# Kernel tuning notes

Measured on AMD Instinct MI355X. Metric: run time of the kernel, lower is better.

## Reference

```python
import jax, jax.numpy as jnp
import numpy as np

B, CM, CT, CA, H, W = 4, 256, 64, 128, 80, 80


def setup_inputs() -> dict:
    key = jax.random.key(0)
    ks = jax.random.split(key, 10)
    s = lambda fan_in: 1.0 / np.sqrt(fan_in)
    return {
        "met_features": jax.random.normal(ks[0], (B, CM, H, W), jnp.float32),
        "terrain_features": jax.random.normal(ks[1], (B, CT, H, W), jnp.float32),
        "wq": jax.random.normal(ks[2], (CA, CM), jnp.float32) * s(CM),
        "bq": jax.random.normal(ks[3], (CA,), jnp.float32) * s(CM),
        "wk": jax.random.normal(ks[4], (CA, CT), jnp.float32) * s(CT),
        "bk": jax.random.normal(ks[5], (CA,), jnp.float32) * s(CT),
        "wv": jax.random.normal(ks[6], (CA, CT), jnp.float32) * s(CT),
        "bv": jax.random.normal(ks[7], (CA,), jnp.float32) * s(CT),
        "wo": jax.random.normal(ks[8], (CM, CA), jnp.float32) * s(CA),
        "bo": jax.random.normal(ks[9], (CM,), jnp.float32) * s(CA),
    }


def reference(met_features, terrain_features, wq, bq, wk, bk, wv, bv, wo, bo):
    b, c, h, w = met_features.shape
    n = h * w  # tokens
    scale = CA ** (-0.5)
    # 1x1 convs == per-pixel linear: [B,Cin,N] -> [B,Cattn,N]
    met = met_features.reshape(b, c, n)
    ter = terrain_features.reshape(b, terrain_features.shape[1], n)
    q = jnp.einsum('oc,bcn->bon', wq, met) + bq[None, :, None]
    k = jnp.einsum('oc,bcn->bon', wk, ter) + bk[None, :, None]
    v = jnp.einsum('oc,bcn->bon', wv, ter) + bv[None, :, None]
    # attn[b, i, j] = sum_c q[b,c,i] * k[b,c,j]
    attn = jax.nn.softmax(jnp.einsum('bci,bcj->bij', q, k) * scale, axis=-1)
    # out[b, c, i] = sum_j v[b,c,j] * attn[b,i,j]
    out = jnp.einsum('bcj,bij->bci', v, attn)
    out = jnp.einsum('oc,bcn->bon', wo, out) + bo[None, :, None]
    return met_features + out.reshape(b, c, h, w)
```

## Files before the change

kernel.cpp:

```cpp
#include <hip/hip_runtime.h>
#include <hip/hip_bf16.h>

#define BB 4
#define CMv 256
#define CTv 64
#define CAv 128
#define NTOK 6400
#define KVSPLIT 5
#define KVRANGE 1280
#define NTILES 20
#define QSCL 0.12753102198064644f

typedef unsigned short u16;
typedef __attribute__((ext_vector_type(8))) short sh8;
typedef __attribute__((ext_vector_type(4))) float f32x4;
typedef __attribute__((ext_vector_type(16))) float f32x16;
typedef __attribute__((ext_vector_type(4))) unsigned uint4v;
typedef __attribute__((ext_vector_type(2))) unsigned uint2v;

__device__ __forceinline__ u16 f2bf(float f) {
  return __builtin_bit_cast(u16, __float2bfloat16(f));
}
__device__ __forceinline__ float bf2f(u16 x) {
  unsigned u = ((unsigned)x) << 16;
  return __builtin_bit_cast(float, u);
}
__device__ __forceinline__ unsigned pk2(float a, float b) {
  return ((unsigned)f2bf(b) << 16) | (unsigned)f2bf(a);
}
__device__ __forceinline__ f32x16 zero16() {
  f32x16 z;
#pragma unroll
  for (int i = 0; i < 16; i++) z[i] = 0.f;
  return z;
}
typedef const __attribute__((address_space(1))) unsigned int* gas_p;
typedef __attribute__((address_space(3))) unsigned int* las_p;
__device__ __forceinline__ void gl_lds16(const u16* g, u16* l) {
  __builtin_amdgcn_global_load_lds((gas_p)g, (las_p)l, 16, 0, 0);
}

__global__ __launch_bounds__(256) void prep(const float* __restrict__ wq,
                                            const float* __restrict__ bq,
                                            const float* __restrict__ wk,
                                            const float* __restrict__ wv,
                                            const float* __restrict__ wo,
                                            u16* __restrict__ wqB,
                                            float* __restrict__ bqs,
                                            u16* __restrict__ wkB,
                                            u16* __restrict__ wvB,
                                            u16* __restrict__ woB) {
  const int i0 = blockIdx.x * 256 + threadIdx.x;
  const int stride = gridDim.x * 256;
  for (int i = i0; i < 128 * 256; i += stride) wqB[i] = f2bf(wq[i] * QSCL);
  for (int i = i0; i < 128 * 64; i += stride) { wkB[i] = f2bf(wk[i]); wvB[i] = f2bf(wv[i]); }
  for (int i = i0; i < 256 * 128; i += stride) woB[i] = f2bf(wo[i]);
  for (int i = i0; i < 128; i += stride) bqs[i] = bq[i] * QSCL;
}

__global__ __launch_bounds__(512, 2) void qkvproj(const float* __restrict__ met,
                                                  const float* __restrict__ ter,
                                                  const u16* __restrict__ wqB,
                                                  const float* __restrict__ bqs,
                                                  const u16* __restrict__ wkB,
                                                  const float* __restrict__ bk,
                                                  const u16* __restrict__ wvB,
                                                  const float* __restrict__ bv,
                                                  u16* __restrict__ Qtm,
                                                  u16* __restrict__ Ktm,
                                                  u16* __restrict__ Vcm) {
  const int tid = threadIdx.x;
  const int w = tid >> 6;
  const int lane = tid & 63;
  const int l31 = lane & 31;
  const int h = lane >> 5;

  if (blockIdx.x < 200) {
    const int b = blockIdx.x / 50;
    const int tokb = (blockIdx.x % 50) * 128;
    const int chg = (w & 3) * 32;
    const int half = w >> 2;
    const u16* wb = wqB + (size_t)(chg + l31) * 256 + h * 8;
    sh8 af[16];
#pragma unroll
    for (int kk = 0; kk < 16; kk++) af[kk] = *(const sh8*)(wb + kk * 16);
    float bias[16];
#pragma unroll
    for (int r = 0; r < 16; r++) bias[r] = bqs[chg + (r & 3) + 8 * (r >> 2) + 4 * h];
    const float* mp = met + (size_t)b * CMv * NTOK;
#pragma unroll
    for (int ct = 0; ct < 2; ct++) {
      const int tok = tokb + (half * 2 + ct) * 32 + l31;
      f32x16 acc = zero16();
#pragma unroll
      for (int kk = 0; kk < 16; kk++) {
        const float* cp = mp + (size_t)(kk * 16 + 8 * h) * NTOK + tok;
        float x0 = cp[0], x1 = cp[(size_t)NTOK], x2 = cp[(size_t)2 * NTOK],
              x3 = cp[(size_t)3 * NTOK], x4 = cp[(size_t)4 * NTOK],
              x5 = cp[(size_t)5 * NTOK], x6 = cp[(size_t)6 * NTOK],
              x7 = cp[(size_t)7 * NTOK];
        uint4v u = {pk2(x0, x1), pk2(x2, x3), pk2(x4, x5), pk2(x6, x7)};
        acc = __builtin_amdgcn_mfma_f32_32x32x16_bf16(
            af[kk], __builtin_bit_cast(sh8, u), acc, 0, 0, 0);
      }
      u16* qp = Qtm + ((size_t)b * NTOK + tok) * CAv;
#pragma unroll
      for (int rq = 0; rq < 4; rq++) {
        const int ch0 = chg + 8 * rq + 4 * h;
        uint2v d = {pk2(acc[4 * rq + 0] + bias[4 * rq + 0],
                        acc[4 * rq + 1] + bias[4 * rq + 1]),
                    pk2(acc[4 * rq + 2] + bias[4 * rq + 2],
                        acc[4 * rq + 3] + bias[4 * rq + 3])};
        *(uint2v*)(qp + ch0) = d;
      }
    }
  } else {
    const int bx = blockIdx.x - 200;
    const int b = bx / 50;
    const int tokb = (bx % 50) * 128;
    const bool isV = w >= 4;
    const int chg = (w & 3) * 32;
    const u16* wb = (isV ? wvB : wkB) + (size_t)(chg + l31) * 64 + h * 8;
    sh8 af[4];
#pragma unroll
    for (int kk = 0; kk < 4; kk++) af[kk] = *(const sh8*)(wb + kk * 16);
    const float* barr = isV ? bv : bk;
    float bias[16];
#pragma unroll
    for (int r = 0; r < 16; r++) bias[r] = barr[chg + (r & 3) + 8 * (r >> 2) + 4 * h];
    const float* tp = ter + (size_t)b * CTv * NTOK;
#pragma unroll
    for (int ct = 0; ct < 4; ct++) {
      const int tok = tokb + ct * 32 + l31;
      f32x16 acc = zero16();
#pragma unroll
      for (int kk = 0; kk < 4; kk++) {
        const float* cp = tp + (size_t)(kk * 16 + 8 * h) * NTOK + tok;
        float x0 = cp[0], x1 = cp[(size_t)NTOK], x2 = cp[(size_t)2 * NTOK],
              x3 = cp[(size_t)3 * NTOK], x4 = cp[(size_t)4 * NTOK],
              x5 = cp[(size_t)5 * NTOK], x6 = cp[(size_t)6 * NTOK],
              x7 = cp[(size_t)7 * NTOK];
        uint4v u = {pk2(x0, x1), pk2(x2, x3), pk2(x4, x5), pk2(x6, x7)};
        acc = __builtin_amdgcn_mfma_f32_32x32x16_bf16(
            af[kk], __builtin_bit_cast(sh8, u), acc, 0, 0, 0);
      }
      if (!isV) {
        u16* kp = Ktm + ((size_t)b * NTOK + tok) * CAv;
#pragma unroll
        for (int rq = 0; rq < 4; rq++) {
          const int ch0 = chg + 8 * rq + 4 * h;
          uint2v d = {pk2(acc[4 * rq + 0] + bias[4 * rq + 0],
                          acc[4 * rq + 1] + bias[4 * rq + 1]),
                      pk2(acc[4 * rq + 2] + bias[4 * rq + 2],
                          acc[4 * rq + 3] + bias[4 * rq + 3])};
          *(uint2v*)(kp + ch0) = d;
        }
      } else {
#pragma unroll
        for (int r = 0; r < 16; r++) {
          const int ch = chg + (r & 3) + 8 * (r >> 2) + 4 * h;
          Vcm[((size_t)b * CAv + ch) * NTOK + tok] = f2bf(acc[r] + bias[r]);
        }
      }
    }
  }
}

__global__ __launch_bounds__(512, 2) void attn(const u16* __restrict__ Qtm,
                                               const u16* __restrict__ Ktm,
                                               const u16* __restrict__ Vcm,
                                               u16* __restrict__ Opart,
                                               float* __restrict__ Lpart) {
  __shared__ __align__(16) unsigned char smem[65536];

  const int tid = threadIdx.x;
  const int w = tid >> 6;
  const int lane = tid & 63;
  const int l31 = lane & 31;
  const int h = lane >> 5;

  const int g = blockIdx.x % 20;
  const int qt = blockIdx.x / 20;
  const int b = g / KVSPLIT;
  const int kvq = g % KVSPLIT;
  const int qb0 = qt * 256;
  const int kv00 = kvq * KVRANGE;

  const u16* Qb = Qtm + ((size_t)b * NTOK + qb0 + w * 32 + l31) * CAv;
  const u16* Kb = Ktm + (size_t)b * NTOK * CAv;
  const u16* Vb = Vcm + (size_t)b * CAv * NTOK;

  sh8 qf[8];
#pragma unroll
  for (int kk = 0; kk < 8; kk++) qf[kk] = *(const sh8*)(Qb + kk * 16 + h * 8);

  const int kr0 = w * 8 + (lane >> 4);
  const int kr1 = kr0 + 4;
  const u16* ksrc0 = Kb + ((size_t)kv00 + kr0) * CAv + (((lane & 15) ^ (kr0 & 15)) * 8);
  const u16* ksrc1 = Kb + ((size_t)kv00 + kr1) * CAv + (((lane & 15) ^ (kr1 & 15)) * 8);
  const int vc = w * 16 + (lane >> 3);
  const u16* vsrc = Vb + (size_t)vc * NTOK + kv00 +
                    (((lane & 7) ^ ((lane >> 3) & 7)) * 8);

  int koff[8];
#pragma unroll
  for (int kk = 0; kk < 8; kk++)
    koff[kk] = l31 * 256 + (((2 * kk + h) ^ (l31 & 15)) << 4);
  int voff[4];
#pragma unroll
  for (int b2 = 0; b2 < 4; b2++)
    voff[b2] = l31 * 128 + (((2 * b2 + h) ^ (l31 & 7)) << 4);

#define STAGE(p)                                               \
  do {                                                         \
    u16* kb_ = (u16*)(smem + (p) * 32768) + w * 1024;          \
    gl_lds16(ksrc0, kb_);                                      \
    gl_lds16(ksrc1, kb_ + 512);                                \
    u16* vb_ = (u16*)(smem + (p) * 32768 + 16384) + w * 1024;  \
    gl_lds16(vsrc, vb_);                                       \
    gl_lds16(vsrc + (size_t)8 * NTOK, vb_ + 512);              \
    ksrc0 += 64 * CAv;                                         \
    ksrc1 += 64 * CAv;                                         \
    vsrc += 64;                                                \
  } while (0)

  STAGE(0);
  asm volatile("s_waitcnt vmcnt(0)" ::: "memory");
  __builtin_amdgcn_s_barrier();

  f32x16 o[4];
#pragma unroll
  for (int i = 0; i < 4; i++) o[i] = zero16();
  float lsum = 0.f;

  int buf = 0;
  for (int t = 0; t < NTILES; t++) {
    if (t < NTILES - 1) STAGE(buf ^ 1);
    const unsigned char* kbuf = smem + buf * 32768;
    const unsigned char* vbuf = kbuf + 16384;
    __builtin_amdgcn_s_setprio(1);
    f32x16 s0 = zero16(), s1 = zero16();
#pragma unroll
    for (int kk = 0; kk < 8; kk++) {
      sh8 kfa = *(const sh8*)(kbuf + koff[kk]);
      sh8 kfb = *(const sh8*)(kbuf + 8192 + koff[kk]);
      s0 = __builtin_amdgcn_mfma_f32_32x32x16_bf16(kfa, qf[kk], s0, 0, 0, 0);
      s1 = __builtin_amdgcn_mfma_f32_32x32x16_bf16(kfb, qf[kk], s1, 0, 0, 0);
    }
    __builtin_amdgcn_s_setprio(0);
    f32x16 p0, p1;
#pragma unroll
    for (int r = 0; r < 16; r++) {
      p0[r] = __builtin_exp2f(s0[r]);
      p1[r] = __builtin_exp2f(s1[r]);
    }
#pragma unroll
    for (int r = 0; r < 16; r++) lsum += p0[r] + p1[r];
    unsigned pkm0[4][2], pkm1[4][2];
#pragma unroll
    for (int rq = 0; rq < 4; rq++) {
      pkm0[rq][0] = pk2(p0[4 * rq + 0], p0[4 * rq + 1]);
      pkm0[rq][1] = pk2(p0[4 * rq + 2], p0[4 * rq + 3]);
      pkm1[rq][0] = pk2(p1[4 * rq + 0], p1[4 * rq + 1]);
      pkm1[rq][1] = pk2(p1[4 * rq + 2], p1[4 * rq + 3]);
    }
#pragma unroll
    for (int x = 0; x < 2; x++) {
#pragma unroll
      for (int b2i = 0; b2i < 2; b2i++) {
        unsigned ow0, ow1, sd0, sd1;
        if (x == 0) {
          ow0 = h ? pkm0[2 * b2i + 1][0] : pkm0[2 * b2i][0];
          ow1 = h ? pkm0[2 * b2i + 1][1] : pkm0[2 * b2i][1];
          sd0 = h ? pkm0[2 * b2i][0] : pkm0[2 * b2i + 1][0];
          sd1 = h ? pkm0[2 * b2i][1] : pkm0[2 * b2i + 1][1];
        } else {
          ow0 = h ? pkm1[2 * b2i + 1][0] : pkm1[2 * b2i][0];
          ow1 = h ? pkm1[2 * b2i + 1][1] : pkm1[2 * b2i][1];
          sd0 = h ? pkm1[2 * b2i][0] : pkm1[2 * b2i + 1][0];
          sd1 = h ? pkm1[2 * b2i][1] : pkm1[2 * b2i + 1][1];
        }
        unsigned rv0 = (unsigned)__shfl_xor((int)sd0, 32);
        unsigned rv1 = (unsigned)__shfl_xor((int)sd1, 32);
        uint4v fw = {h ? rv0 : ow0, h ? rv1 : ow1, h ? ow0 : rv0, h ? ow1 : rv1};
        sh8 pf = __builtin_bit_cast(sh8, fw);
        const int b2 = x * 2 + b2i;
        __builtin_amdgcn_s_setprio(1);
#pragma unroll
        for (int ct = 0; ct < 4; ct++) {
          sh8 vf = *(const sh8*)(vbuf + ct * 4096 + voff[b2]);
          o[ct] = __builtin_amdgcn_mfma_f32_32x32x16_bf16(vf, pf, o[ct], 0, 0, 0);
        }
        __builtin_amdgcn_s_setprio(0);
      }
    }
    asm volatile("s_waitcnt vmcnt(0)" ::: "memory");
    __builtin_amdgcn_s_barrier();
    buf ^= 1;
  }
#undef STAGE

  lsum += __shfl_xor(lsum, 32);
  u16* op = Opart + (((size_t)kvq * BB + b) * NTOK + qb0 + w * 32 + l31) * CAv;
#pragma unroll
  for (int ct = 0; ct < 4; ct++)
#pragma unroll
    for (int rq = 0; rq < 4; rq++) {
      uint2v d = {pk2(o[ct][4 * rq + 0], o[ct][4 * rq + 1]),
                  pk2(o[ct][4 * rq + 2], o[ct][4 * rq + 3])};
      *(uint2v*)(op + ct * 32 + rq * 8 + h * 4) = d;
    }
  if (h == 0) {
    size_t mi = ((size_t)kvq * BB + b) * NTOK + qb0 + w * 32 + l31;
    Lpart[mi] = lsum;
  }
}

__global__ __launch_bounds__(512, 2) void outproj(const float* __restrict__ met,
                                                  const u16* __restrict__ woB,
                                                  const float* __restrict__ bo,
                                                  const u16* __restrict__ Opart,
                                                  const float* __restrict__ Lpart,
                                                  float* __restrict__ out) {
  const int tid = threadIdx.x;
  const int w = tid >> 6;
  const int lane = tid & 63;
  const int l31 = lane & 31;
  const int h = lane >> 5;

  const int b = blockIdx.x / 100;
  const int tokb = (blockIdx.x % 100) * 64;
  const int chg = (w & 3) * 64;
  const int ct = w >> 2;
  const int tok = tokb + ct * 32 + l31;
  const size_t n = (size_t)b * NTOK + tok;
  const size_t PSTR = (size_t)BB * NTOK;

  const u16* wb0 = woB + (size_t)(chg + l31) * 128 + h * 8;
  const u16* wb1 = woB + (size_t)(chg + 32 + l31) * 128 + h * 8;
  sh8 a0[8], a1[8];
#pragma unroll
  for (int kk = 0; kk < 8; kk++) {
    a0[kk] = *(const sh8*)(wb0 + kk * 16);
    a1[kk] = *(const sh8*)(wb1 + kk * 16);
  }

  float L = 0.f;
#pragma unroll
  for (int i = 0; i < KVSPLIT; i++) L += Lpart[i * PSTR + n];
  const float rL = 1.f / L;

  f32x16 acc0 = zero16(), acc1 = zero16();
#pragma unroll
  for (int kk = 0; kk < 8; kk++) {
    float s[8];
#pragma unroll
    for (int j = 0; j < 8; j++) s[j] = 0.f;
#pragma unroll
    for (int i = 0; i < KVSPLIT; i++) {
      sh8 v = *(const sh8*)(Opart + (i * PSTR + n) * CAv + kk * 16 + 8 * h);
#pragma unroll
      for (int j = 0; j < 8; j++) s[j] += bf2f((u16)v[j]);
    }
    uint4v u = {pk2(s[0] * rL, s[1] * rL), pk2(s[2] * rL, s[3] * rL),
                pk2(s[4] * rL, s[5] * rL), pk2(s[6] * rL, s[7] * rL)};
    sh8 bf = __builtin_bit_cast(sh8, u);
    acc0 = __builtin_amdgcn_mfma_f32_32x32x16_bf16(a0[kk], bf, acc0, 0, 0, 0);
    acc1 = __builtin_amdgcn_mfma_f32_32x32x16_bf16(a1[kk], bf, acc1, 0, 0, 0);
  }
#pragma unroll
  for (int r = 0; r < 16; r++) {
    const int ro = (r & 3) + 8 * (r >> 2) + 4 * h;
    const int ch0 = chg + ro;
    const int ch1 = chg + 32 + ro;
    size_t i0 = ((size_t)b * CMv + ch0) * NTOK + tok;
    size_t i1 = ((size_t)b * CMv + ch1) * NTOK + tok;
    out[i0] = met[i0] + acc0[r] + bo[ch0];
    out[i1] = met[i1] + acc1[r] + bo[ch1];
  }
}

extern "C" void kernel_launch(void* const* d_in, const int* in_sizes, int n_in,
                              void* d_out, int out_size, void* d_ws, size_t ws_size,
                              hipStream_t stream) {
  const float* met = (const float*)d_in[0];
  const float* ter = (const float*)d_in[1];
  const float* wq = (const float*)d_in[2];
  const float* bq = (const float*)d_in[3];
  const float* wk = (const float*)d_in[4];
  const float* bk = (const float*)d_in[5];
  const float* wv = (const float*)d_in[6];
  const float* bv = (const float*)d_in[7];
  const float* wo = (const float*)d_in[8];
  const float* bo = (const float*)d_in[9];
  float* out = (float*)d_out;

  u16* Qtm = (u16*)d_ws;
  u16* Ktm = Qtm + (size_t)BB * NTOK * CAv;
  u16* Vcm = Ktm + (size_t)BB * NTOK * CAv;
  u16* Opart = Vcm + (size_t)BB * NTOK * CAv;
  float* Lpart = (float*)(Opart + (size_t)KVSPLIT * BB * NTOK * CAv);
  u16* wqB = (u16*)(Lpart + (size_t)KVSPLIT * BB * NTOK);
  u16* wkB = wqB + 128 * 256;
  u16* wvB = wkB + 128 * 64;
  u16* woB = wvB + 128 * 64;
  float* bqs = (float*)(woB + 256 * 128);

  prep<<<dim3(40), dim3(256), 0, stream>>>(wq, bq, wk, wv, wo, wqB, bqs, wkB, wvB, woB);
  qkvproj<<<dim3(400), dim3(512), 0, stream>>>(met, ter, wqB, bqs, wkB, bk,
                                               wvB, bv, Qtm, Ktm, Vcm);
  attn<<<dim3(500), dim3(512), 0, stream>>>(Qtm, Ktm, Vcm, Opart, Lpart);
  outproj<<<dim3(400), dim3(512), 0, stream>>>(met, woB, bo, Opart, Lpart, out);
}
```

Baseline: 182.3 us.

## Software-pipeline QK^T one tile ahead with triple-buffered K in attention

Restructures the attention loop so the QK^T MFMAs for tile t+1 are issued before the exp/pack/PV work of tile t, letting matrix-core work overlap the softmax VALU work. K is triple-buffered and V double-buffered in LDS, which grows shared memory from 64KB to 80KB. With launch_bounds(512,2), the larger LDS footprint may reduce blocks per CU, and holding an extra pair of score accumulators raises register pressure.

```diff
diff --git a/kernel.cpp b/kernel.cpp
--- a/kernel.cpp
+++ b/kernel.cpp
@@ -171,7 +171,7 @@
                                                const u16* __restrict__ Vcm,
                                                u16* __restrict__ Opart,
                                                float* __restrict__ Lpart) {
-  __shared__ __align__(16) unsigned char smem[65536];
+  __shared__ __align__(16) unsigned char smem[81920];
 
   const int tid = threadIdx.x;
   const int w = tid >> 6;
@@ -211,48 +211,72 @@
   for (int b2 = 0; b2 < 4; b2++)
     voff[b2] = l31 * 128 + (((2 * b2 + h) ^ (l31 & 7)) << 4);
 
-#define STAGE(p)                                               \
-  do {                                                         \
-    u16* kb_ = (u16*)(smem + (p) * 32768) + w * 1024;          \
-    gl_lds16(ksrc0, kb_);                                      \
-    gl_lds16(ksrc1, kb_ + 512);                                \
-    u16* vb_ = (u16*)(smem + (p) * 32768 + 16384) + w * 1024;  \
-    gl_lds16(vsrc, vb_);                                       \
-    gl_lds16(vsrc + (size_t)8 * NTOK, vb_ + 512);              \
-    ksrc0 += 64 * CAv;                                         \
-    ksrc1 += 64 * CAv;                                         \
-    vsrc += 64;                                                \
+#define STAGE_K(p)                                       \
+  do {                                                   \
+    u16* kb_ = (u16*)(smem + (p) * 16384) + w * 1024;    \
+    gl_lds16(ksrc0, kb_);                                \
+    gl_lds16(ksrc1, kb_ + 512);                          \
+    ksrc0 += 64 * CAv;                                   \
+    ksrc1 += 64 * CAv;                                   \
   } while (0)
-
-  STAGE(0);
+#define STAGE_V(v)                                               \
+  do {                                                           \
+    u16* vb_ = (u16*)(smem + 49152 + (v) * 16384) + w * 1024;    \
+    gl_lds16(vsrc, vb_);                                         \
+    gl_lds16(vsrc + (size_t)8 * NTOK, vb_ + 512);                \
+    vsrc += 64;                                                  \
+  } while (0)
+
+  STAGE_K(0);
+  STAGE_V(0);
+  STAGE_K(1);
   asm volatile("s_waitcnt vmcnt(0)" ::: "memory");
   __builtin_amdgcn_s_barrier();
 
-  f32x16 o[4];
-#pragma unroll
-  for (int i = 0; i < 4; i++) o[i] = zero16();
-  float lsum = 0.f;
-
-  int buf = 0;
-  for (int t = 0; t < NTILES; t++) {
-    if (t < NTILES - 1) STAGE(buf ^ 1);
-    const unsigned char* kbuf = smem + buf * 32768;
-    const unsigned char* vbuf = kbuf + 16384;
+  f32x16 sp0 = zero16(), sp1 = zero16();
+  {
+    const unsigned char* kbuf = smem;
     __builtin_amdgcn_s_setprio(1);
-    f32x16 s0 = zero16(), s1 = zero16();
 #pragma unroll
     for (int kk = 0; kk < 8; kk++) {
       sh8 kfa = *(const sh8*)(kbuf + koff[kk]);
       sh8 kfb = *(const sh8*)(kbuf + 8192 + koff[kk]);
-      s0 = __builtin_amdgcn_mfma_f32_32x32x16_bf16(kfa, qf[kk], s0, 0, 0, 0);
-      s1 = __builtin_amdgcn_mfma_f32_32x32x16_bf16(kfb, qf[kk], s1, 0, 0, 0);
+      sp0 = __builtin_amdgcn_mfma_f32_32x32x16_bf16(kfa, qf[kk], sp0, 0, 0, 0);
+      sp1 = __builtin_amdgcn_mfma_f32_32x32x16_bf16(kfb, qf[kk], sp1, 0, 0, 0);
     }
     __builtin_amdgcn_s_setprio(0);
+  }
+
+  f32x16 o[4];
+#pragma unroll
+  for (int i = 0; i < 4; i++) o[i] = zero16();
+  float lsum = 0.f;
+
+  int kqbuf = 1;
+  int ksbuf = 2;
+  for (int t = 0; t < NTILES; t++) {
+    if (t < NTILES - 2) STAGE_K(ksbuf);
+    if (t < NTILES - 1) STAGE_V((t + 1) & 1);
+    f32x16 sn0, sn1;
+    if (t < NTILES - 1) {
+      sn0 = zero16();
+      sn1 = zero16();
+      const unsigned char* kbuf = smem + kqbuf * 16384;
+      __builtin_amdgcn_s_setprio(1);
+#pragma unroll
+      for (int kk = 0; kk < 8; kk++) {
+        sh8 kfa = *(const sh8*)(kbuf + koff[kk]);
+        sh8 kfb = *(const sh8*)(kbuf + 8192 + koff[kk]);
+        sn0 = __builtin_amdgcn_mfma_f32_32x32x16_bf16(kfa, qf[kk], sn0, 0, 0, 0);
+        sn1 = __builtin_amdgcn_mfma_f32_32x32x16_bf16(kfb, qf[kk], sn1, 0, 0, 0);
+      }
+      __builtin_amdgcn_s_setprio(0);
+    }
     f32x16 p0, p1;
 #pragma unroll
     for (int r = 0; r < 16; r++) {
-      p0[r] = __builtin_exp2f(s0[r]);
-      p1[r] = __builtin_exp2f(s1[r]);
+      p0[r] = __builtin_exp2f(sp0[r]);
+      p1[r] = __builtin_exp2f(sp1[r]);
     }
 #pragma unroll
     for (int r = 0; r < 16; r++) lsum += p0[r] + p1[r];
@@ -264,6 +288,7 @@
       pkm1[rq][0] = pk2(p1[4 * rq + 0], p1[4 * rq + 1]);
       pkm1[rq][1] = pk2(p1[4 * rq + 2], p1[4 * rq + 3]);
     }
+    const unsigned char* vbuf = smem + 49152 + (t & 1) * 16384;
 #pragma unroll
     for (int x = 0; x < 2; x++) {
 #pragma unroll
@@ -296,9 +321,15 @@
     }
     asm volatile("s_waitcnt vmcnt(0)" ::: "memory");
     __builtin_amdgcn_s_barrier();
-    buf ^= 1;
-  }
-#undef STAGE
+    if (t < NTILES - 1) {
+      sp0 = sn0;
+      sp1 = sn1;
+    }
+    kqbuf = (kqbuf == 2) ? 0 : kqbuf + 1;
+    ksbuf = (ksbuf == 2) ? 0 : ksbuf + 1;
+  }
+#undef STAGE_K
+#undef STAGE_V
 
   lsum += __shfl_xor(lsum, 32);
   u16* op = Opart + (((size_t)kvq * BB + b) * NTOK + qb0 + w * 32 + l31) * CAv;
```

Result: no change. 184.8 us (+1.4%).
